# Optimization experiments

Hardware: AMD Instinct MI355X
Metric: run time of the kernel (lower is better)

Reference implementation:

```python
import jax, jax.numpy as jnp
import numpy as np

N, D, G, C, M = 4096, 256, 4, 10, 5  # nodes, feat dim, batches, centroids, clusterings


def setup_inputs() -> dict:
    key = jax.random.key(0)
    k1, k2, k3, k4 = jax.random.split(key, 4)
    adj = jax.random.uniform(k1, (N, N), dtype=jnp.float32)
    enc_rep = jax.random.normal(k2, (N, D), dtype=jnp.float32)
    batch_id = jax.random.randint(k3, (N,), 0, G, dtype=jnp.int32)
    cluster_labels = jax.random.randint(k4, (M, N), 0, C, dtype=jnp.int32)
    return {"adj": adj, "enc_rep": enc_rep, "batch_id": batch_id,
            "cluster_labels": cluster_labels, "top_k": 20, "top_k_inter": 10}


def reference(adj, enc_rep, batch_id, cluster_labels, top_k, top_k_inter):
    n = enc_rep.shape[0]
    NEG = jnp.float32(-1e30)
    rows = jnp.arange(n)

    # 'similarity' metric: raw inner-product similarity, full N x N once
    sim = enc_rep @ enc_rep.T                                # [N, N]
    same = batch_id[:, None] == batch_id[None, :]            # same-batch mask

    # intra: top_k+1 within own batch group, drop first (self) column
    intra_sim = jnp.where(same, sim, NEG)
    _, intra_idx = jax.lax.top_k(intra_sim, top_k + 1)
    intra_idx = intra_idx[:, 1:]                              # [N, top_k]

    # inter: top_k_inter among all other batch groups
    inter_sim = jnp.where(same, NEG, sim)
    _, inter_idx = jax.lax.top_k(inter_sim, top_k_inter)      # [N, top_k_inter]

    knn_idx = jnp.concatenate([intra_idx, inter_idx], axis=1)  # [N, k_tot]

    # rep_adj[j, i] = 1 iff j is a knn of i  (coo rows=neighbors, cols=node)
    B = jnp.zeros((n, n), jnp.float32).at[knn_idx, rows[:, None]].set(1.0)
    # common_adj = rep_adj * (rep_adj.T > 0), diag zeroed (mutual-knn graph)
    common = B * B.T
    common = common.at[rows, rows].set(0.0)

    # locality = knn_neighbor * adj
    locality = common * adj

    # padded-neighbor validity mask (I_knn_padded != -1 analog): mutual neighbors
    mutual = common[rows[:, None], knn_idx] > 0               # [N, k_tot]

    # per-clustering close-neighbor test, combined across clusterings
    nb_lbl = cluster_labels[:, knn_idx]                       # [M, N, k_tot]
    eq = cluster_labels[:, :, None] == nb_lbl                 # [M, N, k_tot]
    curr = eq | mutual[None]                                  # curr_close_nei = eq | bool_mask
    all_close = jnp.all(curr, axis=0)                         # AND across clusterings

    return locality, all_close.astype(jnp.float32)
```

## Files before the change

### kernel.cpp

```cpp
#include <hip/hip_runtime.h>
#include <hip/hip_bf16.h>
#include <cfloat>

#define NN 4096
#define DD 256
#define MM 5
#define K_TOT 30
#define TGT_INTRA 32
#define TGT_INTER 24
#define CAND_CAP 64

typedef __attribute__((ext_vector_type(8))) short bf16x8;
typedef __attribute__((ext_vector_type(4))) float f32x4;

__global__ __launch_bounds__(256) void convert_bf16(const float* __restrict__ E,
                                                    ushort* __restrict__ Eb) {
    const int idx = blockIdx.x * 256 + threadIdx.x;
    const float4 f = ((const float4*)E)[idx];
    ushort4 h;
    {
        __hip_bfloat16 a = __float2bfloat16(f.x); h.x = *(ushort*)&a;
        __hip_bfloat16 b = __float2bfloat16(f.y); h.y = *(ushort*)&b;
        __hip_bfloat16 c = __float2bfloat16(f.z); h.z = *(ushort*)&c;
        __hip_bfloat16 d = __float2bfloat16(f.w); h.w = *(ushort*)&d;
    }
    ((ushort4*)Eb)[idx] = h;
}

#define BK 32
#define APITCH 40
#define SPITCH 136

__global__ __launch_bounds__(256) void gemm_bf16(const ushort* __restrict__ Eb,
                                                 ushort* __restrict__ simb) {
    __shared__ union {
        struct { ushort A[128 * APITCH]; ushort B[128 * APITCH]; } s;
        ushort stage[128 * SPITCH];
    } lds;

    const int t = threadIdx.x;
    const int w = t >> 6, lane = t & 63;
    const int quad = lane >> 4, mr = lane & 15;
    const int rowBase = blockIdx.y * 128, colBase = blockIdx.x * 128;
    const int waveRow = (w & 1) * 64, waveCol = (w >> 1) * 64;

    f32x4 acc[4][4];
#pragma unroll
    for (int a = 0; a < 4; ++a)
#pragma unroll
        for (int b = 0; b < 4; ++b) acc[a][b] = (f32x4)(0.0f);

    for (int kc = 0; kc < DD; kc += BK) {
#pragma unroll
        for (int q = 0; q < 2; ++q) {
            const int cid = t * 2 + q;
            const int row = cid >> 2;
            const int ck = (cid & 3) * 8;
            const int4 va = *(const int4*)(Eb + (size_t)(rowBase + row) * DD + kc + ck);
            const int4 vb = *(const int4*)(Eb + (size_t)(colBase + row) * DD + kc + ck);
            *(int4*)(&lds.s.A[row * APITCH + ck]) = va;
            *(int4*)(&lds.s.B[row * APITCH + ck]) = vb;
        }
        __syncthreads();

        bf16x8 af[4], bfr[4];
#pragma unroll
        for (int rt = 0; rt < 4; ++rt)
            af[rt] = *(const bf16x8*)(&lds.s.A[(waveRow + rt * 16 + mr) * APITCH + quad * 8]);
#pragma unroll
        for (int ct = 0; ct < 4; ++ct)
            bfr[ct] = *(const bf16x8*)(&lds.s.B[(waveCol + ct * 16 + mr) * APITCH + quad * 8]);
#pragma unroll
        for (int rt = 0; rt < 4; ++rt)
#pragma unroll
            for (int ct = 0; ct < 4; ++ct)
                acc[rt][ct] = __builtin_amdgcn_mfma_f32_16x16x32_bf16(
                    af[rt], bfr[ct], acc[rt][ct], 0, 0, 0);
        __syncthreads();
    }

#pragma unroll
    for (int rt = 0; rt < 4; ++rt)
#pragma unroll
        for (int ct = 0; ct < 4; ++ct) {
#pragma unroll
            for (int reg = 0; reg < 4; ++reg) {
                const float f = acc[rt][ct][reg];
                __hip_bfloat16 hb = __float2bfloat16(f);
                lds.stage[(waveRow + rt * 16 + quad * 4 + reg) * SPITCH +
                          waveCol + ct * 16 + mr] = *(ushort*)&hb;
            }
        }
    __syncthreads();

#pragma unroll
    for (int it = 0; it < 8; ++it) {
        const int cid = t + it * 256;
        const int row = cid >> 4;
        const int off = (cid & 15) * 8;
        *(int4*)(simb + (size_t)(rowBase + row) * NN + colBase + off) =
            *(const int4*)(&lds.stage[row * SPITCH + off]);
    }
}

__device__ __forceinline__ unsigned f32_sortable(float f) {
    unsigned u = __float_as_uint(f);
    return (u & 0x80000000u) ? ~u : (u | 0x80000000u);
}

__global__ __launch_bounds__(256) void select_rescore(const ushort* __restrict__ sim,
                                                      const float* __restrict__ E,
                                                      const int* __restrict__ batch,
                                                      int* __restrict__ knn) {
    __shared__ unsigned hist[2][2048];
    __shared__ unsigned subhist[2][64];
    __shared__ int Tc[2];
    __shared__ unsigned remc[2];
    __shared__ unsigned thrKey[2];
    __shared__ int candIdx[2][CAND_CAP];
    __shared__ double candVal[2][CAND_CAP];
    __shared__ int cnt[2];
    __shared__ float4 Ei4[DD / 4];

    const int i = blockIdx.x;
    const int t = threadIdx.x;
    const int lane = t & 63;
    const int w = t >> 6;
    const int bi = batch[i];

#pragma unroll
    for (int s = 0; s < 16; ++s) ((unsigned*)hist)[t + s * 256] = 0u;
    if (t < 128) ((unsigned*)subhist)[t] = 0u;
    if (t < 128) ((int*)candIdx)[t] = 0x7FFFFFFF;
    if (t < 2) cnt[t] = 0;
    if (t < 2) { Tc[t] = 0; remc[t] = 1u; }
    if (t < DD / 4) Ei4[t] = ((const float4*)(E + (size_t)i * DD))[t];
    __syncthreads();

    unsigned key[16];
    unsigned mmask = 0;
    const ushort* simRow = sim + (size_t)i * NN;
#pragma unroll
    for (int q = 0; q < 4; ++q) {
        const int j0 = q * 1024 + t * 4;
        const ushort4 sv = *(const ushort4*)(simRow + j0);
        int bv[4];
        *(int4*)bv = *(const int4*)(batch + j0);
        const ushort se[4] = {sv.x, sv.y, sv.z, sv.w};
#pragma unroll
        for (int c = 0; c < 4; ++c) {
            const float f = __uint_as_float((unsigned)se[c] << 16);
            const unsigned k = f32_sortable(f);
            const int u = q * 4 + c;
            key[u] = k;
            const int m = (bv[c] == bi) ? 0 : 1;
            mmask |= (unsigned)m << u;
            atomicAdd(&hist[m][k >> 21], 1u);
        }
    }
    __syncthreads();

    if (w < 2) {
        const int m = w;
        const unsigned target = (m == 0) ? TGT_INTRA : TGT_INTER;
        const int base = (63 - lane) * 32;
        unsigned s = 0;
#pragma unroll
        for (int b = 0; b < 32; ++b) s += hist[m][base + b];
        unsigned cum = s;
        for (int off = 1; off < 64; off <<= 1) {
            const unsigned o = __shfl_up(cum, off);
            if (lane >= off) cum += o;
        }
        if (cum >= target && (cum - s) < target) {
            unsigned excl = cum - s;
            for (int b = base + 31; b >= base; --b) {
                const unsigned h = hist[m][b];
                excl += h;
                if (excl >= target) {
                    Tc[m] = b;
                    remc[m] = target - (excl - h);
                    break;
                }
            }
        }
    }
    __syncthreads();

    const int T0 = Tc[0], T1 = Tc[1];
#pragma unroll
    for (int u = 0; u < 16; ++u) {
        const int m = (mmask >> u) & 1;
        const int T = m ? T1 : T0;
        if ((int)(key[u] >> 21) == T) atomicAdd(&subhist[m][(key[u] >> 15) & 63], 1u);
    }
    __syncthreads();

    if (w < 2) {
        const int m = w;
        const unsigned target2 = remc[m];
        const unsigned s = subhist[m][63 - lane];
        unsigned cum = s;
        for (int off = 1; off < 64; off <<= 1) {
            const unsigned o = __shfl_up(cum, off);
            if (lane >= off) cum += o;
        }
        if (cum >= target2 && (cum - s) < target2)
            thrKey[m] = ((unsigned)Tc[m] << 21) | ((unsigned)(63 - lane) << 15);
    }
    __syncthreads();

    const unsigned thr0 = thrKey[0], thr1 = thrKey[1];
#pragma unroll
    for (int q = 0; q < 4; ++q) {
#pragma unroll
        for (int c = 0; c < 4; ++c) {
            const int u = q * 4 + c;
            const int m = (mmask >> u) & 1;
            if (key[u] >= (m ? thr1 : thr0)) {
                const int pos = atomicAdd(&cnt[m], 1);
                if (pos < CAND_CAP) candIdx[m][pos] = q * 1024 + t * 4 + c;
            }
        }
    }
    __syncthreads();

    if (t < 128) {
        const int m = t >> 6;
        const int slot = t & 63;
        const int c = min(cnt[m], CAND_CAP);
        double val = -DBL_MAX;
        if (slot < c) {
            const int j = candIdx[m][slot];
            const float* ej = E + (size_t)j * DD;
            const float* ei = (const float*)Ei4;
            double a0 = 0, a1 = 0, a2 = 0, a3 = 0;
#pragma unroll 8
            for (int k = 0; k < DD; k += 4) {
                const float4 e = *(const float4*)(ej + k);
                a0 = fma((double)ei[k + 0], (double)e.x, a0);
                a1 = fma((double)ei[k + 1], (double)e.y, a1);
                a2 = fma((double)ei[k + 2], (double)e.z, a2);
                a3 = fma((double)ei[k + 3], (double)e.w, a3);
            }
            val = (a0 + a1) + (a2 + a3);
        }
        candVal[m][slot] = val;
    }
    __syncthreads();

    if (w < 2) {
        const int m = w;
        double val = candVal[m][lane];
        int idx = candIdx[m][lane];
        const int rounds = (m == 0) ? 21 : 10;
        for (int q = 0; q < rounds; ++q) {
            double tv = val;
            int ti = idx;
#pragma unroll
            for (int off = 32; off; off >>= 1) {
                const double ov = __shfl_xor(tv, off);
                const int oi = __shfl_xor(ti, off);
                if (ov > tv || (ov == tv && oi < ti)) { tv = ov; ti = oi; }
            }
            if (lane == 0) {
                if (m == 0) { if (q > 0) knn[i * K_TOT + q - 1] = ti; }
                else        { knn[i * K_TOT + 20 + q] = ti; }
            }
            if (idx == ti) val = -DBL_MAX;
        }
    }
}

__global__ __launch_bounds__(256) void finalize_k(const int* __restrict__ knn,
                                                  const float* __restrict__ adj,
                                                  const int* __restrict__ cl,
                                                  float* __restrict__ out) {
    const int gid = blockIdx.x * 256 + threadIdx.x;
    if (gid >= NN * K_TOT) return;
    const int i = gid / K_TOT;
    const int j = knn[gid];

    bool mutual = false;
#pragma unroll
    for (int s = 0; s < K_TOT; ++s) mutual |= (knn[j * K_TOT + s] == i);

    if (mutual) out[(size_t)i * NN + j] = adj[(size_t)i * NN + j];

    bool ac = mutual;
    if (!ac) {
        bool alleq = true;
#pragma unroll
        for (int m = 0; m < MM; ++m) alleq &= (cl[m * NN + i] == cl[m * NN + j]);
        ac = alleq;
    }
    out[(size_t)NN * NN + gid] = ac ? 1.0f : 0.0f;
}

extern "C" void kernel_launch(void* const* d_in, const int* in_sizes, int n_in,
                              void* d_out, int out_size, void* d_ws, size_t ws_size,
                              hipStream_t stream) {
    const float* adj = (const float*)d_in[0];
    const float* enc = (const float*)d_in[1];
    const int* batch = (const int*)d_in[2];
    const int* cl = (const int*)d_in[3];
    float* out = (float*)d_out;

    const size_t simB = (size_t)NN * NN * sizeof(ushort);
    const size_t ebB = (size_t)NN * DD * sizeof(ushort);
    const size_t knnB = (size_t)NN * K_TOT * sizeof(int);

    const dim3 gGrid(NN / 128, NN / 128);

    if (ws_size >= simB + ebB + knnB) {
        ushort* simb = (ushort*)d_ws;
        ushort* Eb = (ushort*)((char*)d_ws + simB);
        int* knn = (int*)((char*)d_ws + simB + ebB);
        hipMemsetAsync(d_out, 0, (size_t)NN * NN * sizeof(float), stream);
        convert_bf16<<<NN * DD / 4 / 256, 256, 0, stream>>>(enc, Eb);
        gemm_bf16<<<gGrid, 256, 0, stream>>>(Eb, simb);
        select_rescore<<<NN, 256, 0, stream>>>(simb, enc, batch, knn);
        finalize_k<<<(NN * K_TOT + 255) / 256, 256, 0, stream>>>(knn, adj, cl, out);
    } else {
        ushort* simb = (ushort*)d_out;
        ushort* Eb = (ushort*)d_ws;
        int* knn = (int*)((char*)d_ws + ebB);
        convert_bf16<<<NN * DD / 4 / 256, 256, 0, stream>>>(enc, Eb);
        gemm_bf16<<<gGrid, 256, 0, stream>>>(Eb, simb);
        select_rescore<<<NN, 256, 0, stream>>>(simb, enc, batch, knn);
        hipMemsetAsync(d_out, 0, (size_t)NN * NN * sizeof(float), stream);
        finalize_k<<<(NN * K_TOT + 255) / 256, 256, 0, stream>>>(knn, adj, cl, out);
    }
}
```

Measured before the change: 232.3 us.

## Use async global-to-LDS loads with XOR swizzle and a packed 16-bit radix select

The GEMM tile load now uses global_load_lds direct-to-LDS copies into an unpadded, XOR-swizzled layout, replacing register staging plus padded LDS writes. The select kernel is reworked around 16-bit bf16 sortable keys. It uses a single 256-bin histogram with intra and inter counts packed into the low and high 16 bits, then a 256-bin sub-histogram, and each thread reads 16 contiguous elements. The aim is to cut register traffic and LDS footprint in the GEMM, and to shrink histogram clearing and scan work in the select. The risks are 16-bit count overflow in the packed bins and subtle errors in the swizzle or the block-wide scan.

```diff
diff --git a/kernel.cpp b/kernel.cpp
--- a/kernel.cpp
+++ b/kernel.cpp
@@ -13,6 +13,12 @@
 typedef __attribute__((ext_vector_type(8))) short bf16x8;
 typedef __attribute__((ext_vector_type(4))) float f32x4;
 
+__device__ __forceinline__ void async16(const void* g, void* l) {
+    __builtin_amdgcn_global_load_lds((__attribute__((address_space(1))) void*)g,
+                                     (__attribute__((address_space(3))) void*)l,
+                                     16, 0, 0);
+}
+
 __global__ __launch_bounds__(256) void convert_bf16(const float* __restrict__ E,
                                                     ushort* __restrict__ Eb) {
     const int idx = blockIdx.x * 256 + threadIdx.x;
@@ -27,15 +33,11 @@
     ((ushort4*)Eb)[idx] = h;
 }
 
-#define BK 32
-#define APITCH 40
-#define SPITCH 136
-
 __global__ __launch_bounds__(256) void gemm_bf16(const ushort* __restrict__ Eb,
                                                  ushort* __restrict__ simb) {
     __shared__ union {
-        struct { ushort A[128 * APITCH]; ushort B[128 * APITCH]; } s;
-        ushort stage[128 * SPITCH];
+        struct { ushort A[128 * 32]; ushort B[128 * 32]; } s;
+        ushort stage[128 * 136];
     } lds;
 
     const int t = threadIdx.x;
@@ -44,32 +46,37 @@
     const int rowBase = blockIdx.y * 128, colBase = blockIdx.x * 128;
     const int waveRow = (w & 1) * 64, waveCol = (w >> 1) * 64;
 
+    const int lrow = lane >> 2;
+    const int lslot = lane & 3;
+    const int gchunk = lslot ^ ((lrow >> 1) & 3);
+
     f32x4 acc[4][4];
 #pragma unroll
     for (int a = 0; a < 4; ++a)
 #pragma unroll
         for (int b = 0; b < 4; ++b) acc[a][b] = (f32x4)(0.0f);
 
-    for (int kc = 0; kc < DD; kc += BK) {
-#pragma unroll
-        for (int q = 0; q < 2; ++q) {
-            const int cid = t * 2 + q;
-            const int row = cid >> 2;
-            const int ck = (cid & 3) * 8;
-            const int4 va = *(const int4*)(Eb + (size_t)(rowBase + row) * DD + kc + ck);
-            const int4 vb = *(const int4*)(Eb + (size_t)(colBase + row) * DD + kc + ck);
-            *(int4*)(&lds.s.A[row * APITCH + ck]) = va;
-            *(int4*)(&lds.s.B[row * APITCH + ck]) = vb;
+    for (int kc = 0; kc < DD; kc += 32) {
+#pragma unroll
+        for (int n = 0; n < 2; ++n) {
+            const int r = w * 32 + n * 16 + lrow;
+            const ushort* ga = Eb + (size_t)(rowBase + r) * DD + kc + gchunk * 8;
+            const ushort* gb = Eb + (size_t)(colBase + r) * DD + kc + gchunk * 8;
+            async16(ga, &lds.s.A[(w * 32 + n * 16) * 32]);
+            async16(gb, &lds.s.B[(w * 32 + n * 16) * 32]);
         }
         __syncthreads();
 
+        const int swzF = (mr >> 1) & 3;
         bf16x8 af[4], bfr[4];
 #pragma unroll
         for (int rt = 0; rt < 4; ++rt)
-            af[rt] = *(const bf16x8*)(&lds.s.A[(waveRow + rt * 16 + mr) * APITCH + quad * 8]);
+            af[rt] = *(const bf16x8*)&lds.s.A[(waveRow + rt * 16 + mr) * 32 +
+                                              ((quad ^ swzF) * 8)];
 #pragma unroll
         for (int ct = 0; ct < 4; ++ct)
-            bfr[ct] = *(const bf16x8*)(&lds.s.B[(waveCol + ct * 16 + mr) * APITCH + quad * 8]);
+            bfr[ct] = *(const bf16x8*)&lds.s.B[(waveCol + ct * 16 + mr) * 32 +
+                                               ((quad ^ swzF) * 8)];
 #pragma unroll
         for (int rt = 0; rt < 4; ++rt)
 #pragma unroll
@@ -82,39 +89,32 @@
 #pragma unroll
     for (int rt = 0; rt < 4; ++rt)
 #pragma unroll
-        for (int ct = 0; ct < 4; ++ct) {
+        for (int ct = 0; ct < 4; ++ct)
 #pragma unroll
             for (int reg = 0; reg < 4; ++reg) {
-                const float f = acc[rt][ct][reg];
-                __hip_bfloat16 hb = __float2bfloat16(f);
-                lds.stage[(waveRow + rt * 16 + quad * 4 + reg) * SPITCH +
+                __hip_bfloat16 hb = __float2bfloat16(acc[rt][ct][reg]);
+                lds.stage[(waveRow + rt * 16 + quad * 4 + reg) * 136 +
                           waveCol + ct * 16 + mr] = *(ushort*)&hb;
             }
-        }
-    __syncthreads();
-
+    __syncthreads();
 #pragma unroll
     for (int it = 0; it < 8; ++it) {
         const int cid = t + it * 256;
         const int row = cid >> 4;
         const int off = (cid & 15) * 8;
         *(int4*)(simb + (size_t)(rowBase + row) * NN + colBase + off) =
-            *(const int4*)(&lds.stage[row * SPITCH + off]);
-    }
-}
-
-__device__ __forceinline__ unsigned f32_sortable(float f) {
-    unsigned u = __float_as_uint(f);
-    return (u & 0x80000000u) ? ~u : (u | 0x80000000u);
+            *(const int4*)&lds.stage[row * 136 + off];
+    }
 }
 
 __global__ __launch_bounds__(256) void select_rescore(const ushort* __restrict__ sim,
                                                       const float* __restrict__ E,
                                                       const int* __restrict__ batch,
                                                       int* __restrict__ knn) {
-    __shared__ unsigned hist[2][2048];
-    __shared__ unsigned subhist[2][64];
-    __shared__ int Tc[2];
+    __shared__ unsigned hist[256];
+    __shared__ unsigned subhist[256];
+    __shared__ unsigned wsum[4];
+    __shared__ int cb[2];
     __shared__ unsigned remc[2];
     __shared__ unsigned thrKey[2];
     __shared__ int candIdx[2][CAND_CAP];
@@ -128,98 +128,107 @@
     const int w = t >> 6;
     const int bi = batch[i];
 
-#pragma unroll
-    for (int s = 0; s < 16; ++s) ((unsigned*)hist)[t + s * 256] = 0u;
-    if (t < 128) ((unsigned*)subhist)[t] = 0u;
+    hist[t] = 0u;
+    subhist[t] = 0u;
     if (t < 128) ((int*)candIdx)[t] = 0x7FFFFFFF;
-    if (t < 2) cnt[t] = 0;
-    if (t < 2) { Tc[t] = 0; remc[t] = 1u; }
+    if (t < 2) { cnt[t] = 0; cb[t] = 0; remc[t] = 1u; thrKey[t] = 0u; }
     if (t < DD / 4) Ei4[t] = ((const float4*)(E + (size_t)i * DD))[t];
     __syncthreads();
 
-    unsigned key[16];
+    unsigned short key[16];
     unsigned mmask = 0;
-    const ushort* simRow = sim + (size_t)i * NN;
-#pragma unroll
-    for (int q = 0; q < 4; ++q) {
-        const int j0 = q * 1024 + t * 4;
-        const ushort4 sv = *(const ushort4*)(simRow + j0);
-        int bv[4];
-        *(int4*)bv = *(const int4*)(batch + j0);
-        const ushort se[4] = {sv.x, sv.y, sv.z, sv.w};
-#pragma unroll
-        for (int c = 0; c < 4; ++c) {
-            const float f = __uint_as_float((unsigned)se[c] << 16);
-            const unsigned k = f32_sortable(f);
-            const int u = q * 4 + c;
-            key[u] = k;
+    {
+        const ushort* sp = sim + (size_t)i * NN + t * 16;
+        const int4 s0 = *(const int4*)sp;
+        const int4 s1 = *(const int4*)(sp + 8);
+        const unsigned sw[8] = {(unsigned)s0.x, (unsigned)s0.y, (unsigned)s0.z,
+                                (unsigned)s0.w, (unsigned)s1.x, (unsigned)s1.y,
+                                (unsigned)s1.z, (unsigned)s1.w};
+        const int* bp = batch + t * 16;
+        int bv[16];
+        *(int4*)&bv[0] = *(const int4*)bp;
+        *(int4*)&bv[4] = *(const int4*)(bp + 4);
+        *(int4*)&bv[8] = *(const int4*)(bp + 8);
+        *(int4*)&bv[12] = *(const int4*)(bp + 12);
+#pragma unroll
+        for (int c = 0; c < 16; ++c) {
+            const unsigned u = (sw[c >> 1] >> ((c & 1) * 16)) & 0xFFFFu;
+            const unsigned k = (u & 0x8000u) ? (u ^ 0xFFFFu) : (u | 0x8000u);
+            key[c] = (unsigned short)k;
             const int m = (bv[c] == bi) ? 0 : 1;
-            mmask |= (unsigned)m << u;
-            atomicAdd(&hist[m][k >> 21], 1u);
-        }
-    }
-    __syncthreads();
-
-    if (w < 2) {
-        const int m = w;
-        const unsigned target = (m == 0) ? TGT_INTRA : TGT_INTER;
-        const int base = (63 - lane) * 32;
-        unsigned s = 0;
-#pragma unroll
-        for (int b = 0; b < 32; ++b) s += hist[m][base + b];
-        unsigned cum = s;
+            mmask |= (unsigned)m << c;
+            atomicAdd(&hist[k >> 8], m ? 0x10000u : 1u);
+        }
+    }
+    __syncthreads();
+
+    {
+        const int b = 255 - t;
+        const unsigned h = hist[b];
+        unsigned cum = h;
         for (int off = 1; off < 64; off <<= 1) {
             const unsigned o = __shfl_up(cum, off);
             if (lane >= off) cum += o;
         }
-        if (cum >= target && (cum - s) < target) {
-            unsigned excl = cum - s;
-            for (int b = base + 31; b >= base; --b) {
-                const unsigned h = hist[m][b];
-                excl += h;
-                if (excl >= target) {
-                    Tc[m] = b;
-                    remc[m] = target - (excl - h);
-                    break;
-                }
-            }
-        }
-    }
-    __syncthreads();
-
-    const int T0 = Tc[0], T1 = Tc[1];
-#pragma unroll
-    for (int u = 0; u < 16; ++u) {
-        const int m = (mmask >> u) & 1;
-        const int T = m ? T1 : T0;
-        if ((int)(key[u] >> 21) == T) atomicAdd(&subhist[m][(key[u] >> 15) & 63], 1u);
-    }
-    __syncthreads();
-
-    if (w < 2) {
-        const int m = w;
-        const unsigned target2 = remc[m];
-        const unsigned s = subhist[m][63 - lane];
-        unsigned cum = s;
+        if (lane == 63) wsum[w] = cum;
+        __syncthreads();
+        unsigned add = 0;
+        for (int ww = 0; ww < w; ++ww) add += wsum[ww];
+        cum += add;
+        const unsigned cI = cum & 0xFFFFu, hI = h & 0xFFFFu;
+        const unsigned cT = cum >> 16, hT = h >> 16;
+        if (cI >= TGT_INTRA && cI - hI < TGT_INTRA) {
+            cb[0] = b;
+            remc[0] = TGT_INTRA - (cI - hI);
+        }
+        if (cT >= TGT_INTER && cT - hT < TGT_INTER) {
+            cb[1] = b;
+            remc[1] = TGT_INTER - (cT - hT);
+        }
+    }
+    __syncthreads();
+
+    {
+        const int cb0 = cb[0], cb1 = cb[1];
+#pragma unroll
+        for (int c = 0; c < 16; ++c) {
+            const int m = (mmask >> c) & 1;
+            if ((int)(key[c] >> 8) == (m ? cb1 : cb0))
+                atomicAdd(&subhist[key[c] & 0xFF], m ? 0x10000u : 1u);
+        }
+    }
+    __syncthreads();
+
+    {
+        const unsigned rI = remc[0], rT = remc[1];
+        const int cb0 = cb[0], cb1 = cb[1];
+        const int b = 255 - t;
+        const unsigned h = subhist[b];
+        unsigned cum = h;
         for (int off = 1; off < 64; off <<= 1) {
             const unsigned o = __shfl_up(cum, off);
             if (lane >= off) cum += o;
         }
-        if (cum >= target2 && (cum - s) < target2)
-            thrKey[m] = ((unsigned)Tc[m] << 21) | ((unsigned)(63 - lane) << 15);
-    }
-    __syncthreads();
-
-    const unsigned thr0 = thrKey[0], thr1 = thrKey[1];
-#pragma unroll
-    for (int q = 0; q < 4; ++q) {
-#pragma unroll
-        for (int c = 0; c < 4; ++c) {
-            const int u = q * 4 + c;
-            const int m = (mmask >> u) & 1;
-            if (key[u] >= (m ? thr1 : thr0)) {
+        if (lane == 63) wsum[w] = cum;
+        __syncthreads();
+        unsigned add = 0;
+        for (int ww = 0; ww < w; ++ww) add += wsum[ww];
+        cum += add;
+        const unsigned cI = cum & 0xFFFFu, hI = h & 0xFFFFu;
+        const unsigned cT = cum >> 16, hT = h >> 16;
+        if (cI >= rI && cI - hI < rI) thrKey[0] = ((unsigned)cb0 << 8) | (unsigned)b;
+        if (cT >= rT && cT - hT < rT) thrKey[1] = ((unsigned)cb1 << 8) | (unsigned)b;
+    }
+    __syncthreads();
+
+    {
+        const unsigned thr0 = thrKey[0], thr1 = thrKey[1];
+#pragma unroll
+        for (int c = 0; c < 16; ++c) {
+            const int m = (mmask >> c) & 1;
+            if ((unsigned)key[c] >= (m ? thr1 : thr0)) {
                 const int pos = atomicAdd(&cnt[m], 1);
-                if (pos < CAND_CAP) candIdx[m][pos] = q * 1024 + t * 4 + c;
+                if (pos < CAND_CAP) candIdx[m][pos] = t * 16 + c;
             }
         }
     }
```

New measurement: 227.2 us. 2.2% less time.
